# Kernel optimization log

Measured on AMD Instinct MI355X. Metric: run time of the kernel, lower is better.

Reference implementation:

```python
import jax, jax.numpy as jnp
import numpy as np

B, N, DM = 4, 1024, 256
DEPTH, D_STATE, D_CONV, EXPAND = 12, 16, 4, 2
D_INNER = EXPAND * DM
DT_RANK = (DM + 15) // 16
MASKED = 256            # fixed number of masked tokens per row (CLS never masked)
MAX_VIS = N - MASKED    # static visible length -> jit-safe gather/pad
EPS = 1e-5


def setup_inputs() -> dict:
    key = jax.random.key(0)
    ks = jax.random.split(key, 8)
    tokens = jax.random.normal(ks[0], (B, N, DM), jnp.float32)
    # mask: exactly MASKED random positions True per row, among first N-1 (CLS visible)
    def row_mask(k):
        perm = jax.random.permutation(k, N - 1)
        return jnp.zeros((N,), bool).at[perm[:MASKED]].set(True)
    mask = jax.vmap(row_mask)(jax.random.split(ks[1], B))
    sc = 0.02
    L = DEPTH
    in_proj_w = jax.random.normal(ks[2], (L, 2 * D_INNER, DM), jnp.float32) * sc
    conv_w = jax.random.normal(ks[3], (L, D_INNER, D_CONV), jnp.float32) * sc
    conv_b = jnp.zeros((L, D_INNER), jnp.float32)
    x_proj_w = jax.random.normal(ks[4], (L, DT_RANK + 2 * D_STATE, D_INNER), jnp.float32) * sc
    dt_proj_w = jax.random.normal(ks[5], (L, D_INNER, DT_RANK), jnp.float32) * (DT_RANK ** -0.5)
    dt_proj_b = jnp.full((L, D_INNER), float(np.log(np.expm1(0.01))), jnp.float32)  # softplus^-1(0.01)
    A_log = jnp.log(jnp.broadcast_to(jnp.arange(1, D_STATE + 1, dtype=jnp.float32), (L, D_INNER, D_STATE)))
    D_skip = jnp.ones((L, D_INNER), jnp.float32)
    out_proj_w = jax.random.normal(ks[6], (L, DM, D_INNER), jnp.float32) * sc
    norm_w = jnp.ones((L, DM), jnp.float32)
    norm_f_w = jnp.ones((DM,), jnp.float32)
    ln_w = jnp.ones((DM,), jnp.float32)
    ln_b = jnp.zeros((DM,), jnp.float32)
    return dict(tokens=tokens, mask=mask, in_proj_w=in_proj_w, conv_w=conv_w, conv_b=conv_b,
                x_proj_w=x_proj_w, dt_proj_w=dt_proj_w, dt_proj_b=dt_proj_b, A_log=A_log,
                D_skip=D_skip, out_proj_w=out_proj_w, norm_w=norm_w, norm_f_w=norm_f_w,
                ln_w=ln_w, ln_b=ln_b)


def _rmsnorm(x, w):
    return x * jax.lax.rsqrt(jnp.mean(x * x, axis=-1, keepdims=True) + EPS) * w


def _selective_scan(dA, dBu, C):
    # linear recurrence h_t = dA_t * h_{t-1} + dBu_t via associative scan over time
    def comb(l, r):
        return (r[0] * l[0], r[0] * l[1] + r[1])
    _, h = jax.lax.associative_scan(comb, (dA, dBu), axis=1)  # [B,L,d_inner,d_state]
    return jnp.einsum('blds,bls->bld', h, C)


def _mamba(h, p):
    in_w, cw, cb, xw, dtw, dtb, Alog, Dd, ow = p
    L = h.shape[1]
    xz = jnp.einsum('bld,ed->ble', h, in_w)           # [B,L,2*d_inner]
    x, z = jnp.split(xz, 2, axis=-1)
    # causal depthwise conv1d (torch Conv1d, padding=d_conv-1, truncated to L)
    xp = jnp.pad(x, ((0, 0), (D_CONV - 1, 0), (0, 0)))
    x = sum(xp[:, k:k + L, :] * cw[:, k] for k in range(D_CONV)) + cb
    x = jax.nn.silu(x)
    xdbl = jnp.einsum('bld,ed->ble', x, xw)           # [B,L,dt_rank+2*d_state]
    dtr = xdbl[..., :DT_RANK]
    Bm = xdbl[..., DT_RANK:DT_RANK + D_STATE]
    Cm = xdbl[..., DT_RANK + D_STATE:]
    dt = jax.nn.softplus(jnp.einsum('blr,dr->bld', dtr, dtw) + dtb)  # [B,L,d_inner]
    A = -jnp.exp(Alog)                                 # [d_inner,d_state]
    dA = jnp.exp(dt[..., None] * A)                    # [B,L,d_inner,d_state]
    dBu = (dt * x)[..., None] * Bm[:, :, None, :]
    y = _selective_scan(dA, dBu, Cm) + Dd * x
    y = y * jax.nn.silu(z)
    return jnp.einsum('bld,od->blo', y, ow)


def _forward(tokens, mask, in_proj_w, conv_w, conv_b, x_proj_w, dt_proj_w, dt_proj_b,
             A_log, D_skip, out_proj_w, norm_w, norm_f_w, ln_w, ln_b):
    # gather visible tokens, preserving order (stable sort: visible first)
    sort_key = mask.astype(jnp.int32) * N + jnp.arange(N)
    order = jnp.argsort(sort_key, axis=1)[:, :MAX_VIS]           # [B,MAX_VIS]
    vis = jnp.take_along_axis(tokens, order[..., None], axis=1)  # [B,MAX_VIS,DM]

    def step(carry, p):
        hidden, residual = carry
        residual = hidden + residual
        hidden = _mamba(_rmsnorm(residual, p[0]), p[1:])
        return (hidden, residual), None

    layer_params = (norm_w, in_proj_w, conv_w, conv_b, x_proj_w, dt_proj_w, dt_proj_b,
                    A_log, D_skip, out_proj_w)
    (h, r), _ = jax.lax.scan(step, (vis, jnp.zeros_like(vis)), layer_params)
    h = _rmsnorm(h + r, norm_f_w)
    # final nn.LayerNorm
    mu = jnp.mean(h, axis=-1, keepdims=True)
    var = jnp.mean((h - mu) ** 2, axis=-1, keepdims=True)
    h = (h - mu) * jax.lax.rsqrt(var + EPS) * ln_w + ln_b
    return h[:, :-1], h[:, -1]


def reference(tokens, mask, in_proj_w, conv_w, conv_b, x_proj_w, dt_proj_w, dt_proj_b,
              A_log, D_skip, out_proj_w, norm_w, norm_f_w, ln_w, ln_b):
    return _forward(tokens, mask, in_proj_w, conv_w, conv_b, x_proj_w, dt_proj_w, dt_proj_b,
                    A_log, D_skip, out_proj_w, norm_w, norm_f_w, ln_w, ln_b)
```

## Files before the change

kernel.cpp:

```cpp
#include <hip/hip_runtime.h>
#include <stdint.h>

#define B_ 4
#define N_TOK 1024
#define DM 256
#define DEPTH 12
#define DSTATE 16
#define DIN 512
#define LVIS 768
#define MROWS (B_ * LVIS)
#define NCHUNK 64
#define CLEN 12
#define EPS_F 1e-5f
#define YS 520
#define AS_ 264
#define LOG2E 1.4426950408889634f
#define LN2   0.6931471805599453f

typedef __attribute__((ext_vector_type(8))) short s8v;
typedef __attribute__((ext_vector_type(4))) float f4v;

__device__ __forceinline__ float bs2f(uint32_t u) {
  uint32_t x = (u & 0xffffu) << 16;
  float f; __builtin_memcpy(&f, &x, 4); return f;
}
__device__ __forceinline__ uint16_t f2b(float f) {
  uint32_t u; __builtin_memcpy(&u, &f, 4);
  return (uint16_t)((u + 0x7fffu + ((u >> 16) & 1u)) >> 16);
}
__device__ __forceinline__ float exp2_f(float x) {
  float r; asm("v_exp_f32 %0, %1" : "=v"(r) : "v"(x)); return r;
}
__device__ __forceinline__ float log2_f(float x) {
  float r; asm("v_log_f32 %0, %1" : "=v"(r) : "v"(x)); return r;
}
__device__ __forceinline__ float rcp_f(float x) {
  float r; asm("v_rcp_f32 %0, %1" : "=v"(r) : "v"(x)); return r;
}
__device__ __forceinline__ float silu_f(float x) {
  return x * rcp_f(1.f + exp2_f(-x * LOG2E));
}
__device__ __forceinline__ float softplus_f(float x) {
  float t = exp2_f(-fabsf(x) * LOG2E);
  return fmaxf(x, 0.f) + log2_f(1.f + t) * LN2;
}
__device__ __forceinline__ float block_sum256(float v, volatile float* scr) {
  int t = threadIdx.x, lane = t & 63, wid = t >> 6;
#pragma unroll
  for (int o = 32; o > 0; o >>= 1) v += __shfl_down(v, o);
  __syncthreads();
  if (lane == 0) scr[wid] = v;
  __syncthreads();
  return scr[0] + scr[1] + scr[2] + scr[3];
}

__global__ void detect_kernel(const void* mask, const uint32_t* nf, int* flags) {
  __shared__ int cnt[3];
  int t = threadIdx.x;
  if (t < 3) cnt[t] = 0;
  __syncthreads();
  const uint32_t* pi = (const uint32_t*)mask;
  const uint16_t* ph = (const uint16_t*)mask;
  const uint8_t*  pb = (const uint8_t*)mask;
  int c32 = 0, cbf = 0, c8 = 0;
  for (int i = t; i < 1024; i += 256) {
    c32 += (pi[i] != 0u);
    cbf += (ph[i] != 0);
    c8  += (pb[i] != 0);
  }
  atomicAdd(&cnt[0], c32);
  atomicAdd(&cnt[1], cbf);
  atomicAdd(&cnt[2], c8);
  __syncthreads();
  if (t == 0) {
    int f;
    if (cnt[0] == 256) f = 0;
    else if (cnt[1] == 256) f = 2;
    else f = 1;
    flags[0] = f;
    flags[1] = (nf[0] == 0x3F800000u) ? 0 : 1;
  }
}

struct CvtArgs {
  const void* src[13];
  void*       dst[13];
  int         n[13];
  int         isb16[13];
};
__global__ __launch_bounds__(256) void cvt_all_kernel(CvtArgs a, int total,
                                                      const int* __restrict__ flags) {
  int e = blockIdx.x * 256 + threadIdx.x;
  if (e >= total) return;
  int i = 0;
  while (e >= a.n[i]) { e -= a.n[i]; ++i; }
  int srcb16 = flags[1];
  if (a.isb16[i]) {
    uint16_t v = srcb16 ? ((const uint16_t*)a.src[i])[e]
                        : f2b(((const float*)a.src[i])[e]);
    ((uint16_t*)a.dst[i])[e] = v;
  } else {
    float v = srcb16 ? bs2f(((const uint16_t*)a.src[i])[e])
                     : ((const float*)a.src[i])[e];
    ((float*)a.dst[i])[e] = v;
  }
}

__global__ __launch_bounds__(1024) void order_kernel(const void* mask,
                                                     const int* __restrict__ flags,
                                                     int* __restrict__ order) {
  int b = blockIdx.x, i = threadIdx.x;
  int f = flags[0];
  int mv;
  if (f == 0)      mv = (((const uint32_t*)mask)[b * N_TOK + i] != 0u);
  else if (f == 1) mv = (((const uint8_t*)mask)[b * N_TOK + i] != 0);
  else             mv = (((const uint16_t*)mask)[b * N_TOK + i] != 0);
  int vis = !mv;
  unsigned long long mb = __ballot(vis);
  int lane = i & 63, wid = i >> 6;
  int wpre = __popcll(mb & ((1ull << lane) - 1ull));
  __shared__ int wsum[16];
  __shared__ int woff[16];
  if (lane == 0) wsum[wid] = __popcll(mb);
  __syncthreads();
  if (i == 0) { int a = 0; for (int w = 0; w < 16; ++w) { woff[w] = a; a += wsum[w]; } }
  __syncthreads();
  if (vis) {
    int pos = woff[wid] + wpre;
    if (pos < LVIS) order[b * LVIS + pos] = i;
  }
}

__global__ __launch_bounds__(256) void gather_rms_kernel(const void* __restrict__ tokens,
                                                         const int* __restrict__ order,
                                                         const int* __restrict__ flags,
                                                         const float* __restrict__ nw,
                                                         float* __restrict__ residual,
                                                         uint16_t* __restrict__ rmsb16) {
  __shared__ float scr[4];
  int row = blockIdx.x;
  int b = row / LVIS;
  int d = threadIdx.x;
  int idx = order[row];
  size_t src = ((size_t)(b * N_TOK + idx)) * DM + d;
  float v = flags[1] ? bs2f(((const uint16_t*)tokens)[src]) : ((const float*)tokens)[src];
  size_t i = (size_t)row * DM + d;
  residual[i] = v;
  float ss = block_sum256(v * v, scr);
  rmsb16[i] = f2b(v * rsqrtf(ss / DM + EPS_F) * nw[d]);
}

__device__ __forceinline__ size_t cidx(int b, int c, int s, int d) {
  return (((size_t)(b * NCHUNK + c) * 16 + s)) * DIN + d;
}

__global__ __launch_bounds__(1024, 4) void scan1_kernel(
    const uint16_t* __restrict__ rmsb16, const uint16_t* __restrict__ inw,
    const uint16_t* __restrict__ xw,
    const float* __restrict__ cw, const float* __restrict__ cb,
    const float* __restrict__ dtw, const float* __restrict__ dtb,
    const float* __restrict__ Alog, const float* __restrict__ Dsk,
    uint16_t* __restrict__ zh16, float* __restrict__ hend,
    float* __restrict__ pend, float* __restrict__ xdbl_out,
    float* __restrict__ yloc, float* __restrict__ Ssum) {
  __shared__ uint16_t As[16 * AS_];
  __shared__ uint16_t xzl[16 * YS];
  __shared__ float red[8][768];
  __shared__ float xds[CLEN * 48];
  uint16_t* zt = (uint16_t*)red;
  const int t = threadIdx.x;
  const int wv = t >> 6, lane = t & 63;
  const int lm = lane & 15, lq = lane >> 4;
  const int c = blockIdx.x & (NCHUNK - 1);
  const int b = blockIdx.x >> 6;
  const int rowbase = b * LVIS + c * CLEN;
  if (t < 512) {
    int r = t >> 5, seg = t & 31;
    int grow = rowbase - 3 + r;
    if (grow < 0) grow = 0;
    if (grow > MROWS - 1) grow = MROWS - 1;
    *(uint4*)(As + r * AS_ + seg * 8) =
        *(const uint4*)(rmsb16 + (size_t)grow * DM + seg * 8);
  }
  __syncthreads();
  {
    f4v acc[4];
#pragma unroll
    for (int j = 0; j < 4; ++j) acc[j] = (f4v){0.f, 0.f, 0.f, 0.f};
    for (int k0 = 0; k0 < DM; k0 += 32) {
      s8v a = *(const s8v*)(As + lm * AS_ + k0 + lq * 8);
#pragma unroll
      for (int j = 0; j < 4; ++j) {
        int n = (4 * wv + j) * 16 + lm;
        s8v bw = *(const s8v*)(inw + (size_t)n * DM + k0 + lq * 8);
        acc[j] = __builtin_amdgcn_mfma_f32_16x16x32_bf16(a, bw, acc[j], 0, 0, 0);
      }
    }
#pragma unroll
    for (int j = 0; j < 4; ++j) {
      int col = (4 * wv + j) * 16 + lm;
#pragma unroll
      for (int rr = 0; rr < 4; ++rr) {
        int tr = lq * 4 + rr;
        uint16_t v = f2b(acc[j][rr]);
        if (col < 512) xzl[tr * YS + col] = v;
        else           zt[tr * YS + (col - 512)] = v;
      }
    }
  }
  __syncthreads();
  if (t < 768) {
    int r = t >> 6, q = t & 63;
    *(uint4*)(zh16 + (size_t)(rowbase + r) * 512 + q * 8) =
        *(const uint4*)(zt + (3 + r) * YS + q * 8);
  }
  __syncthreads();
  if (wv < 8) {
    f4v acc[3];
#pragma unroll
    for (int j = 0; j < 3; ++j) acc[j] = (f4v){0.f, 0.f, 0.f, 0.f};
    const int l = c * CLEN + lm;
    const bool t3 = l >= 3, t2 = l >= 2, t1 = l >= 1;
#pragma unroll
    for (int ki = 0; ki < 2; ++ki) {
      int kk = wv * 64 + ki * 32 + lq * 8;
      s8v a8 = {0, 0, 0, 0, 0, 0, 0, 0};
      if (lm < CLEN) {
        const s8v zv = {0, 0, 0, 0, 0, 0, 0, 0};
        s8v x0 = *(const s8v*)(xzl + (lm + 3) * YS + kk);
        s8v x1 = t1 ? *(const s8v*)(xzl + (lm + 2) * YS + kk) : zv;
        s8v x2 = t2 ? *(const s8v*)(xzl + (lm + 1) * YS + kk) : zv;
        s8v x3 = t3 ? *(const s8v*)(xzl + (lm + 0) * YS + kk) : zv;
#pragma unroll
        for (int j = 0; j < 8; ++j) {
          int ch = kk + j;
          float4 w = *(const float4*)(cw + ch * 4);
          float a = cb[ch] + bs2f((uint16_t)x3[j]) * w.x +
                    bs2f((uint16_t)x2[j]) * w.y +
                    bs2f((uint16_t)x1[j]) * w.z + bs2f((uint16_t)x0[j]) * w.w;
          a8[j] = (short)f2b(silu_f(a));
        }
      }
#pragma unroll
      for (int j = 0; j < 3; ++j) {
        s8v bb = *(const s8v*)(xw + (size_t)(j * 16 + lm) * DIN + kk);
        acc[j] = __builtin_amdgcn_mfma_f32_16x16x32_bf16(a8, bb, acc[j], 0, 0, 0);
      }
    }
#pragma unroll
    for (int j = 0; j < 3; ++j)
#pragma unroll
      for (int rr = 0; rr < 4; ++rr)
        red[wv][(lq * 4 + rr) * 48 + j * 16 + lm] = acc[j][rr];
  }
  __syncthreads();
  if (t < CLEN * 48) {
    float v = red[0][t] + red[1][t] + red[2][t] + red[3][t] +
              red[4][t] + red[5][t] + red[6][t] + red[7][t];
    xds[t] = v;
    xdbl_out[(size_t)(rowbase + t / 48) * 48 + (t % 48)] = v;
  }
  __syncthreads();
  if (t < DIN) {
    const int d = t;
    float A2[16], dw[16];
    {
      const float4* ap = (const float4*)(Alog + (size_t)d * 16);
      const float4* wp = (const float4*)(dtw + (size_t)d * 16);
#pragma unroll
      for (int q = 0; q < 4; ++q) {
        float4 a4 = ap[q], w4 = wp[q];
        A2[4 * q + 0] = -__expf(a4.x) * LOG2E;
        A2[4 * q + 1] = -__expf(a4.y) * LOG2E;
        A2[4 * q + 2] = -__expf(a4.z) * LOG2E;
        A2[4 * q + 3] = -__expf(a4.w) * LOG2E;
        dw[4 * q + 0] = w4.x; dw[4 * q + 1] = w4.y;
        dw[4 * q + 2] = w4.z; dw[4 * q + 3] = w4.w;
      }
    }
    float dtbv = dtb[d], cbv = cb[d], Dv = Dsk[d];
    float4 cwv = *(const float4*)(cw + d * 4);
    float w3 = 0.f, w2 = 0.f, w1 = 0.f;
    if (c > 0) {
      w3 = bs2f(xzl[0 * YS + d]);
      w2 = bs2f(xzl[1 * YS + d]);
      w1 = bs2f(xzl[2 * YS + d]);
    }
    float h[16];
#pragma unroll
    for (int s = 0; s < 16; ++s) h[s] = 0.f;
    float S = 0.f;
    for (int l = 0; l < CLEN; ++l) {
      float xn = bs2f(xzl[(l + 3) * YS + d]);
      float xv = silu_f(cbv + w3 * cwv.x + w2 * cwv.y + w1 * cwv.z + xn * cwv.w);
      w3 = w2; w2 = w1; w1 = xn;
      const float* xd = xds + l * 48;
      float dtraw = dtbv;
#pragma unroll
      for (int q = 0; q < 16; ++q) dtraw += xd[q] * dw[q];
      float dtv = softplus_f(dtraw);
      float dtx = dtv * xv;
      S += dtv;
      float y = 0.f;
#pragma unroll
      for (int s = 0; s < 16; ++s) {
        float dA = exp2_f(dtv * A2[s]);
        h[s] = dA * h[s] + dtx * xd[16 + s];
        y += h[s] * xd[32 + s];
      }
      size_t oi = (size_t)(rowbase + l) * DIN + d;
      yloc[oi] = y + Dv * xv;
      Ssum[oi] = S;
    }
#pragma unroll
    for (int s = 0; s < 16; ++s) {
      hend[cidx(b, c, s, d)] = h[s];
      pend[cidx(b, c, s, d)] = exp2_f(A2[s] * S);
    }
  }
}

__global__ __launch_bounds__(256) void scan2_kernel(const float* __restrict__ hend,
                                                    const float* __restrict__ pend,
                                                    float* __restrict__ hin) {
  __shared__ float sP[4 * 64];
  __shared__ float sE[4 * 64];
  int t = threadIdx.x;
  int w = t >> 6, lane = t & 63;
  int chain = blockIdx.x * 64 + lane;
  int d = chain & (DIN - 1);
  int s = (chain >> 9) & 15;
  int b = chain >> 13;
  float P = 1.f, E = 0.f;
  float pr[16], hr[16];
#pragma unroll
  for (int i = 0; i < 16; ++i) {
    size_t idx = cidx(b, w * 16 + i, s, d);
    float pv = pend[idx], ev = hend[idx];
    pr[i] = pv; hr[i] = ev;
    E = pv * E + ev;
    P *= pv;
  }
  sP[w * 64 + lane] = P;
  sE[w * 64 + lane] = E;
  __syncthreads();
  float hc = 0.f;
#pragma unroll
  for (int j = 0; j < 3; ++j)
    if (j < w) hc = sP[j * 64 + lane] * hc + sE[j * 64 + lane];
#pragma unroll
  for (int i = 0; i < 16; ++i) {
    hin[cidx(b, w * 16 + i, s, d)] = hc;
    hc = pr[i] * hc + hr[i];
  }
}

__global__ __launch_bounds__(1024, 4) void scan3_fused_kernel(
    const uint16_t* __restrict__ zh16, const float* __restrict__ xdbl,
    const float* __restrict__ Alog, const float* __restrict__ hin,
    const float* __restrict__ yloc, const float* __restrict__ Ssum,
    const uint16_t* __restrict__ W, const float* __restrict__ nw,
    float* __restrict__ residual, uint16_t* __restrict__ rmsb16) {
  __shared__ float xds[CLEN * 48];
  __shared__ uint16_t yml[16 * YS];
  __shared__ float part[16][16];
  __shared__ float scale[16];
  const int t = threadIdx.x;
  const int c = blockIdx.x & (NCHUNK - 1);
  const int b = blockIdx.x >> 6;
  const int rowbase = b * LVIS + c * CLEN;
  if (t < CLEN * 48)
    xds[t] = xdbl[(size_t)(rowbase + t / 48) * 48 + (t % 48)];
  for (int e = t; e < 4 * 512; e += 1024)
    yml[(12 + (e >> 9)) * YS + (e & 511)] = 0;
  __syncthreads();
  if (t < DIN) {
    const int d = t;
    float A2[16];
    {
      const float4* ap = (const float4*)(Alog + (size_t)d * 16);
#pragma unroll
      for (int q = 0; q < 4; ++q) {
        float4 a4 = ap[q];
        A2[4 * q + 0] = -__expf(a4.x) * LOG2E;
        A2[4 * q + 1] = -__expf(a4.y) * LOG2E;
        A2[4 * q + 2] = -__expf(a4.z) * LOG2E;
        A2[4 * q + 3] = -__expf(a4.w) * LOG2E;
      }
    }
    float chin[16];
#pragma unroll
    for (int s = 0; s < 16; ++s) chin[s] = hin[cidx(b, c, s, d)];
    for (int l = 0; l < CLEN; ++l) {
      int row = rowbase + l;
      size_t oi = (size_t)row * DIN + d;
      float S = Ssum[oi];
      float yl = yloc[oi];
      const float* xd = xds + l * 48;
      float carry = 0.f;
#pragma unroll
      for (int s = 0; s < 16; ++s)
        carry += xd[32 + s] * chin[s] * exp2_f(A2[s] * S);
      float zv = bs2f(zh16[(size_t)row * 512 + d]);
      yml[l * YS + d] = f2b((yl + carry) * silu_f(zv));
    }
  }
  __syncthreads();
  {
    const int wv = t >> 6, lane = t & 63;
    const int lm = lane & 15, lq = lane >> 4;
    f4v acc = (f4v){0.f, 0.f, 0.f, 0.f};
    for (int k0 = 0; k0 < DIN; k0 += 32) {
      s8v a = *(const s8v*)(yml + lm * YS + k0 + lq * 8);
      int n = wv * 16 + lm;
      s8v bf = *(const s8v*)(W + (size_t)n * DIN + k0 + lq * 8);
      acc = __builtin_amdgcn_mfma_f32_16x16x32_bf16(a, bf, acc, 0, 0, 0);
    }
    float vv[4];
    float sum[4] = {0.f, 0.f, 0.f, 0.f};
#pragma unroll
    for (int rr = 0; rr < 4; ++rr) {
      int row = lq * 4 + rr;
      if (row < CLEN) {
        int col = wv * 16 + lm;
        float v = acc[rr] + residual[(size_t)(rowbase + row) * DM + col];
        vv[rr] = v;
        sum[rr] += v * v;
      }
    }
#pragma unroll
    for (int rr = 0; rr < 4; ++rr) {
#pragma unroll
      for (int o = 1; o < 16; o <<= 1) sum[rr] += __shfl_xor(sum[rr], o);
    }
    if (lm == 0) {
#pragma unroll
      for (int rr = 0; rr < 4; ++rr) {
        int row = lq * 4 + rr;
        if (row < 16) part[row][wv] = sum[rr];
      }
    }
    __syncthreads();
    if (t < CLEN) {
      float s = 0.f;
#pragma unroll
      for (int w = 0; w < 16; ++w) s += part[t][w];
      scale[t] = rsqrtf(s / DM + EPS_F);
    }
    __syncthreads();
#pragma unroll
    for (int rr = 0; rr < 4; ++rr) {
      int row = lq * 4 + rr;
      if (row < CLEN) {
        float sc = scale[row];
        int col = wv * 16 + lm;
        float v = vv[rr];
        size_t oi = (size_t)(rowbase + row) * DM + col;
        residual[oi] = v;
        rmsb16[oi] = f2b(v * sc * nw[col]);
      }
    }
  }
}

__global__ __launch_bounds__(256) void final_kernel(const float* __restrict__ residual,
                                                    const float* __restrict__ nfw,
                                                    const float* __restrict__ lnw,
                                                    const float* __restrict__ lnb,
                                                    const int* __restrict__ flags,
                                                    void* __restrict__ out) {
  __shared__ float scr[4];
  int row = blockIdx.x, d = threadIdx.x;
  size_t i = (size_t)row * DM + d;
  float v = residual[i];
  float ss = block_sum256(v * v, scr);
  float h = v * rsqrtf(ss / DM + EPS_F) * nfw[d];
  float mu = block_sum256(h, scr) / DM;
  float dv = h - mu;
  float var = block_sum256(dv * dv, scr) / DM;
  float o = dv * rsqrtf(var + EPS_F) * lnw[d] + lnb[d];
  int b = row / LVIS, l = row % LVIS;
  size_t oi = (l < LVIS - 1)
                ? ((size_t)(b * (LVIS - 1) + l) * DM + d)
                : ((size_t)B_ * (LVIS - 1) * DM + (size_t)b * DM + d);
  if (flags[1]) ((uint16_t*)out)[oi] = f2b(o);
  else          ((float*)out)[oi] = o;
}

extern "C" void kernel_launch(void* const* d_in, const int* in_sizes, int n_in,
                              void* d_out, int out_size, void* d_ws, size_t ws_size,
                              hipStream_t stream) {
  char* ws = (char*)d_ws;
  size_t off = 0;
  auto alloc = [&](size_t bytes) -> void* {
    void* p = ws + off;
    off += (bytes + 255) & ~(size_t)255;
    return p;
  };
  const int f32_idx[10] = {3, 4, 6, 7, 8, 9, 11, 12, 13, 14};
  const int b16_idx[3]  = {2, 5, 10};
  float*    f32c[15] = {nullptr};
  uint16_t* b16c[15] = {nullptr};
  for (int j = 0; j < 10; ++j) {
    int i = f32_idx[j];
    f32c[i] = (float*)alloc((size_t)in_sizes[i] * 4);
  }
  for (int j = 0; j < 3; ++j) {
    int i = b16_idx[j];
    b16c[i] = (uint16_t*)alloc((size_t)in_sizes[i] * 2);
  }
  float*    residual = (float*)alloc((size_t)MROWS * DM * 4);
  uint16_t* rmsb16   = (uint16_t*)alloc((size_t)MROWS * DM * 2);
  uint16_t* zh16     = (uint16_t*)alloc((size_t)MROWS * 512 * 2);
  float*    xdbl     = (float*)alloc((size_t)MROWS * 48 * 4);
  float*    hend     = (float*)alloc((size_t)B_ * NCHUNK * DIN * 16 * 4);
  float*    pend     = (float*)alloc((size_t)B_ * NCHUNK * DIN * 16 * 4);
  float*    hin      = (float*)alloc((size_t)B_ * NCHUNK * DIN * 16 * 4);
  float*    yloc     = (float*)alloc((size_t)MROWS * DIN * 4);
  float*    Ssum     = (float*)alloc((size_t)MROWS * DIN * 4);
  int*      order    = (int*)alloc((size_t)B_ * LVIS * 4);
  int*      flags    = (int*)alloc(256);

  detect_kernel<<<1, 256, 0, stream>>>(d_in[1], (const uint32_t*)d_in[12], flags);

  CvtArgs ca;
  int total = 0, slot = 0;
  for (int j = 0; j < 3; ++j) {
    int i = b16_idx[j];
    ca.src[slot] = d_in[i]; ca.dst[slot] = b16c[i];
    ca.n[slot] = in_sizes[i]; ca.isb16[slot] = 1;
    total += in_sizes[i]; ++slot;
  }
  for (int j = 0; j < 10; ++j) {
    int i = f32_idx[j];
    ca.src[slot] = d_in[i]; ca.dst[slot] = f32c[i];
    ca.n[slot] = in_sizes[i]; ca.isb16[slot] = 0;
    total += in_sizes[i]; ++slot;
  }
  cvt_all_kernel<<<(total + 255) / 256, 256, 0, stream>>>(ca, total, flags);

  const uint16_t* in_w   = b16c[2];
  const float*    conv_w = f32c[3];
  const float*    conv_b = f32c[4];
  const uint16_t* x_w    = b16c[5];
  const float*    dt_w   = f32c[6];
  const float*    dt_b   = f32c[7];
  const float*    A_log  = f32c[8];
  const float*    D_skip = f32c[9];
  const uint16_t* out_w  = b16c[10];
  const float*    norm_w = f32c[11];
  const float*    norm_f = f32c[12];
  const float*    ln_w   = f32c[13];
  const float*    ln_b   = f32c[14];

  order_kernel<<<B_, 1024, 0, stream>>>(d_in[1], flags, order);
  gather_rms_kernel<<<MROWS, 256, 0, stream>>>(d_in[0], order, flags, norm_w,
                                               residual, rmsb16);

  for (int L = 0; L < DEPTH; ++L) {
    scan1_kernel<<<B_ * NCHUNK, 1024, 0, stream>>>(
        rmsb16, in_w + (size_t)L * 1024 * DM, x_w + (size_t)L * 48 * DIN,
        conv_w + (size_t)L * DIN * 4, conv_b + (size_t)L * DIN,
        dt_w + (size_t)L * DIN * 16, dt_b + (size_t)L * DIN,
        A_log + (size_t)L * DIN * 16, D_skip + (size_t)L * DIN,
        zh16, hend, pend, xdbl, yloc, Ssum);
    scan2_kernel<<<(B_ * 16 * DIN * 4) / 256, 256, 0, stream>>>(hend, pend, hin);
    int Lnext = (L + 1 < DEPTH) ? (L + 1) : L;
    scan3_fused_kernel<<<B_ * NCHUNK, 1024, 0, stream>>>(
        zh16, xdbl, A_log + (size_t)L * DIN * 16, hin, yloc, Ssum,
        out_w + (size_t)L * DM * DIN, norm_w + (size_t)Lnext * DM,
        residual, rmsb16);
  }

  final_kernel<<<MROWS, 256, 0, stream>>>(residual, norm_f, ln_w, ln_b,
                                          flags, d_out);
}
```

Measured before the change: 788.5 us.

## Split scan states across thread pairs, recompute chunk decay, fuse final norm into last layer

In scan1, each channel's 16 SSM states are now split across two threads, so all 1024 threads run the scan instead of 512; the partial y values are combined with a lane shuffle. The pend buffer is removed, and scan2 recomputes each chunk's decay from Ssum and A_log. The xdbl buffer now stores only the 16 C columns. The final RMSNorm+LayerNorm kernel is folded into a templated last-layer variant of scan3, which drops one launch and one pass over the residual. The costs are extra exp work in scan2, a duplicated dt projection in each thread pair, and more syncs in the last layer.

```diff
diff --git a/kernel.cpp b/kernel.cpp
--- a/kernel.cpp
+++ b/kernel.cpp
@@ -161,8 +161,8 @@
     const float* __restrict__ dtw, const float* __restrict__ dtb,
     const float* __restrict__ Alog, const float* __restrict__ Dsk,
     uint16_t* __restrict__ zh16, float* __restrict__ hend,
-    float* __restrict__ pend, float* __restrict__ xdbl_out,
-    float* __restrict__ yloc, float* __restrict__ Ssum) {
+    float* __restrict__ xdbl_out, float* __restrict__ yloc,
+    float* __restrict__ Ssum) {
   __shared__ uint16_t As[16 * AS_];
   __shared__ uint16_t xzl[16 * YS];
   __shared__ float red[8][768];
@@ -258,22 +258,29 @@
     float v = red[0][t] + red[1][t] + red[2][t] + red[3][t] +
               red[4][t] + red[5][t] + red[6][t] + red[7][t];
     xds[t] = v;
-    xdbl_out[(size_t)(rowbase + t / 48) * 48 + (t % 48)] = v;
-  }
-  __syncthreads();
-  if (t < DIN) {
-    const int d = t;
-    float A2[16], dw[16];
+    int k = t % 48;
+    if (k >= 32)
+      xdbl_out[(size_t)(rowbase + t / 48) * 16 + (k - 32)] = v;
+  }
+  __syncthreads();
+  {
+    const int d = t >> 1;
+    const int s0 = (t & 1) * 8;
+    float A2[8], dw[16];
     {
-      const float4* ap = (const float4*)(Alog + (size_t)d * 16);
+      const float4* ap = (const float4*)(Alog + (size_t)d * 16 + s0);
       const float4* wp = (const float4*)(dtw + (size_t)d * 16);
 #pragma unroll
-      for (int q = 0; q < 4; ++q) {
-        float4 a4 = ap[q], w4 = wp[q];
+      for (int q = 0; q < 2; ++q) {
+        float4 a4 = ap[q];
         A2[4 * q + 0] = -__expf(a4.x) * LOG2E;
         A2[4 * q + 1] = -__expf(a4.y) * LOG2E;
         A2[4 * q + 2] = -__expf(a4.z) * LOG2E;
         A2[4 * q + 3] = -__expf(a4.w) * LOG2E;
+      }
+#pragma unroll
+      for (int q = 0; q < 4; ++q) {
+        float4 w4 = wp[q];
         dw[4 * q + 0] = w4.x; dw[4 * q + 1] = w4.y;
         dw[4 * q + 2] = w4.z; dw[4 * q + 3] = w4.w;
       }
@@ -286,9 +293,9 @@
       w2 = bs2f(xzl[1 * YS + d]);
       w1 = bs2f(xzl[2 * YS + d]);
     }
-    float h[16];
-#pragma unroll
-    for (int s = 0; s < 16; ++s) h[s] = 0.f;
+    float h[8];
+#pragma unroll
+    for (int i = 0; i < 8; ++i) h[i] = 0.f;
     float S = 0.f;
     for (int l = 0; l < CLEN; ++l) {
       float xn = bs2f(xzl[(l + 3) * YS + d]);
@@ -303,25 +310,27 @@
       S += dtv;
       float y = 0.f;
 #pragma unroll
-      for (int s = 0; s < 16; ++s) {
-        float dA = exp2_f(dtv * A2[s]);
-        h[s] = dA * h[s] + dtx * xd[16 + s];
-        y += h[s] * xd[32 + s];
-      }
-      size_t oi = (size_t)(rowbase + l) * DIN + d;
-      yloc[oi] = y + Dv * xv;
-      Ssum[oi] = S;
-    }
-#pragma unroll
-    for (int s = 0; s < 16; ++s) {
-      hend[cidx(b, c, s, d)] = h[s];
-      pend[cidx(b, c, s, d)] = exp2_f(A2[s] * S);
-    }
+      for (int i = 0; i < 8; ++i) {
+        float dA = exp2_f(dtv * A2[i]);
+        h[i] = dA * h[i] + dtx * xd[16 + s0 + i];
+        y += h[i] * xd[32 + s0 + i];
+      }
+      y += __shfl_xor(y, 1);
+      if (!(t & 1)) {
+        size_t oi = (size_t)(rowbase + l) * DIN + d;
+        yloc[oi] = y + Dv * xv;
+        Ssum[oi] = S;
+      }
+    }
+#pragma unroll
+    for (int i = 0; i < 8; ++i)
+      hend[cidx(b, c, s0 + i, d)] = h[i];
   }
 }
 
 __global__ __launch_bounds__(256) void scan2_kernel(const float* __restrict__ hend,
-                                                    const float* __restrict__ pend,
+                                                    const float* __restrict__ Ssum,
+                                                    const float* __restrict__ Alog,
                                                     float* __restrict__ hin) {
   __shared__ float sP[4 * 64];
   __shared__ float sE[4 * 64];
@@ -331,12 +340,15 @@
   int d = chain & (DIN - 1);
   int s = (chain >> 9) & 15;
   int b = chain >> 13;
+  float A2v = -__expf(Alog[(size_t)d * 16 + s]) * LOG2E;
   float P = 1.f, E = 0.f;
   float pr[16], hr[16];
 #pragma unroll
   for (int i = 0; i < 16; ++i) {
-    size_t idx = cidx(b, w * 16 + i, s, d);
-    float pv = pend[idx], ev = hend[idx];
+    int cc = w * 16 + i;
+    float Send = Ssum[(size_t)(b * LVIS + cc * CLEN + CLEN - 1) * DIN + d];
+    float pv = exp2_f(A2v * Send);
+    float ev = hend[cidx(b, cc, s, d)];
     pr[i] = pv; hr[i] = ev;
     E = pv * E + ev;
     P *= pv;
@@ -355,13 +367,17 @@
   }
 }
 
+template <int LAST>
 __global__ __launch_bounds__(1024, 4) void scan3_fused_kernel(
     const uint16_t* __restrict__ zh16, const float* __restrict__ xdbl,
     const float* __restrict__ Alog, const float* __restrict__ hin,
     const float* __restrict__ yloc, const float* __restrict__ Ssum,
     const uint16_t* __restrict__ W, const float* __restrict__ nw,
-    float* __restrict__ residual, uint16_t* __restrict__ rmsb16) {
-  __shared__ float xds[CLEN * 48];
+    float* __restrict__ residual, uint16_t* __restrict__ rmsb16,
+    const float* __restrict__ nfw, const float* __restrict__ lnw,
+    const float* __restrict__ lnb, const int* __restrict__ flags,
+    void* __restrict__ out) {
+  __shared__ float xds[CLEN * 16];
   __shared__ uint16_t yml[16 * YS];
   __shared__ float part[16][16];
   __shared__ float scale[16];
@@ -369,8 +385,8 @@
   const int c = blockIdx.x & (NCHUNK - 1);
   const int b = blockIdx.x >> 6;
   const int rowbase = b * LVIS + c * CLEN;
-  if (t < CLEN * 48)
-    xds[t] = xdbl[(size_t)(rowbase + t / 48) * 48 + (t % 48)];
+  if (t < CLEN * 16)
+    xds[t] = xdbl[(size_t)(rowbase + t / 16) * 16 + (t % 16)];
   for (int e = t; e < 4 * 512; e += 1024)
     yml[(12 + (e >> 9)) * YS + (e & 511)] = 0;
   __syncthreads();
@@ -396,11 +412,11 @@
       size_t oi = (size_t)row * DIN + d;
       float S = Ssum[oi];
       float yl = yloc[oi];
-      const float* xd = xds + l * 48;
+      const float* xd = xds + l * 16;
       float carry = 0.f;
 #pragma unroll
       for (int s = 0; s < 16; ++s)
-        carry += xd[32 + s] * chin[s] * exp2_f(A2[s] * S);
+        carry += xd[s] * chin[s] * exp2_f(A2[s] * S);
       float zv = bs2f(zh16[(size_t)row * 512 + d]);
       yml[l * YS + d] = f2b((yl + carry) * silu_f(zv));
     }
@@ -409,10 +425,11 @@
   {
     const int wv = t >> 6, lane = t & 63;
     const int lm = lane & 15, lq = lane >> 4;
+    const int col = wv * 16 + lm;
     f4v acc = (f4v){0.f, 0.f, 0.f, 0.f};
     for (int k0 = 0; k0 < DIN; k0 += 32) {
       s8v a = *(const s8v*)(yml + lm * YS + k0 + lq * 8);
-      int n = wv * 16 + lm;
+      int n = col;
       s8v bf = *(const s8v*)(W + (size_t)n * DIN + k0 + lq * 8);
       acc = __builtin_amdgcn_mfma_f32_16x16x32_bf16(a, bf, acc, 0, 0, 0);
     }
@@ -422,7 +439,6 @@
     for (int rr = 0; rr < 4; ++rr) {
       int row = lq * 4 + rr;
       if (row < CLEN) {
-        int col = wv * 16 + lm;
         float v = acc[rr] + residual[(size_t)(rowbase + row) * DM + col];
         vv[rr] = v;
         sum[rr] += v * v;
@@ -448,43 +464,99 @@
       scale[t] = rsqrtf(s / DM + EPS_F);
     }
     __syncthreads();
-#pragma unroll
-    for (int rr = 0; rr < 4; ++rr) {
-      int row = lq * 4 + rr;
-      if (row < CLEN) {
-        float sc = scale[row];
-        int col = wv * 16 + lm;
-        float v = vv[rr];
-        size_t oi = (size_t)(rowbase + row) * DM + col;
-        residual[oi] = v;
-        rmsb16[oi] = f2b(v * sc * nw[col]);
-      }
-    }
-  }
-}
-
-__global__ __launch_bounds__(256) void final_kernel(const float* __restrict__ residual,
-                                                    const float* __restrict__ nfw,
-                                                    const float* __restrict__ lnw,
-                                                    const float* __restrict__ lnb,
-                                                    const int* __restrict__ flags,
-                                                    void* __restrict__ out) {
-  __shared__ float scr[4];
-  int row = blockIdx.x, d = threadIdx.x;
-  size_t i = (size_t)row * DM + d;
-  float v = residual[i];
-  float ss = block_sum256(v * v, scr);
-  float h = v * rsqrtf(ss / DM + EPS_F) * nfw[d];
-  float mu = block_sum256(h, scr) / DM;
-  float dv = h - mu;
-  float var = block_sum256(dv * dv, scr) / DM;
-  float o = dv * rsqrtf(var + EPS_F) * lnw[d] + lnb[d];
-  int b = row / LVIS, l = row % LVIS;
-  size_t oi = (l < LVIS - 1)
-                ? ((size_t)(b * (LVIS - 1) + l) * DM + d)
-                : ((size_t)B_ * (LVIS - 1) * DM + (size_t)b * DM + d);
-  if (flags[1]) ((uint16_t*)out)[oi] = f2b(o);
-  else          ((float*)out)[oi] = o;
+    if (!LAST) {
+#pragma unroll
+      for (int rr = 0; rr < 4; ++rr) {
+        int row = lq * 4 + rr;
+        if (row < CLEN) {
+          float sc = scale[row];
+          float v = vv[rr];
+          size_t oi = (size_t)(rowbase + row) * DM + col;
+          residual[oi] = v;
+          rmsb16[oi] = f2b(v * sc * nw[col]);
+        }
+      }
+    } else {
+      float hv[4];
+      float mu[4] = {0.f, 0.f, 0.f, 0.f};
+#pragma unroll
+      for (int rr = 0; rr < 4; ++rr) {
+        int row = lq * 4 + rr;
+        hv[rr] = 0.f;
+        if (row < CLEN) {
+          hv[rr] = vv[rr] * scale[row] * nfw[col];
+          mu[rr] = hv[rr];
+        }
+      }
+#pragma unroll
+      for (int rr = 0; rr < 4; ++rr) {
+#pragma unroll
+        for (int o = 1; o < 16; o <<= 1) mu[rr] += __shfl_xor(mu[rr], o);
+      }
+      __syncthreads();
+      if (lm == 0) {
+#pragma unroll
+        for (int rr = 0; rr < 4; ++rr) {
+          int row = lq * 4 + rr;
+          if (row < 16) part[row][wv] = mu[rr];
+        }
+      }
+      __syncthreads();
+      if (t < CLEN) {
+        float s = 0.f;
+#pragma unroll
+        for (int w = 0; w < 16; ++w) s += part[t][w];
+        scale[t] = s / DM;
+      }
+      __syncthreads();
+      float dv_[4];
+      float va[4] = {0.f, 0.f, 0.f, 0.f};
+#pragma unroll
+      for (int rr = 0; rr < 4; ++rr) {
+        int row = lq * 4 + rr;
+        dv_[rr] = 0.f;
+        if (row < CLEN) {
+          dv_[rr] = hv[rr] - scale[row];
+          va[rr] = dv_[rr] * dv_[rr];
+        }
+      }
+#pragma unroll
+      for (int rr = 0; rr < 4; ++rr) {
+#pragma unroll
+        for (int o = 1; o < 16; o <<= 1) va[rr] += __shfl_xor(va[rr], o);
+      }
+      __syncthreads();
+      if (lm == 0) {
+#pragma unroll
+        for (int rr = 0; rr < 4; ++rr) {
+          int row = lq * 4 + rr;
+          if (row < 16) part[row][wv] = va[rr];
+        }
+      }
+      __syncthreads();
+      if (t < CLEN) {
+        float s = 0.f;
+#pragma unroll
+        for (int w = 0; w < 16; ++w) s += part[t][w];
+        scale[t] = rsqrtf(s / DM + EPS_F);
+      }
+      __syncthreads();
+      int f1 = flags[1];
+#pragma unroll
+      for (int rr = 0; rr < 4; ++rr) {
+        int row = lq * 4 + rr;
+        if (row < CLEN) {
+          float o = dv_[rr] * scale[row] * lnw[col] + lnb[col];
+          int l2 = c * CLEN + row;
+          size_t oi = (l2 < LVIS - 1)
+                        ? ((size_t)(b * (LVIS - 1) + l2) * DM + col)
+                        : ((size_t)B_ * (LVIS - 1) * DM + (size_t)b * DM + col);
+          if (f1) ((uint16_t*)out)[oi] = f2b(o);
+          else    ((float*)out)[oi] = o;
+        }
+      }
+    }
+  }
 }
 
 extern "C" void kernel_launch(void* const* d_in, const int* in_sizes, int n_in,
@@ -512,9 +584,8 @@
   float*    residual = (float*)alloc((size_t)MROWS * DM * 4);
   uint16_t* rmsb16   = (uint16_t*)alloc((size_t)MROWS * DM * 2);
   uint16_t* zh16     = (uint16_t*)alloc((size_t)MROWS * 512 * 2);
-  float*    xdbl     = (float*)alloc((size_t)MROWS * 48 * 4);
+  float*    xdbl     = (float*)alloc((size_t)MROWS * 16 * 4);
   float*    hend     = (float*)alloc((size_t)B_ * NCHUNK * DIN * 16 * 4);
-  float*    pend     = (float*)alloc((size_t)B_ * NCHUNK * DIN * 16 * 4);
   float*    hin      = (float*)alloc((size_t)B_ * NCHUNK * DIN * 16 * 4);
   float*    yloc     = (float*)alloc((size_t)MROWS * DIN * 4);
   float*    Ssum     = (float*)alloc((size_t)MROWS * DIN * 4);
@@ -563,15 +634,20 @@
         conv_w + (size_t)L * DIN * 4, conv_b + (size_t)L * DIN,
         dt_w + (size_t)L * DIN * 16, dt_b + (size_t)L * DIN,
         A_log + (size_t)L * DIN * 16, D_skip + (size_t)L * DIN,
-        zh16, hend, pend, xdbl, yloc, Ssum);
-    scan2_kernel<<<(B_ * 16 * DIN * 4) / 256, 256, 0, stream>>>(hend, pend, hin);
+        zh16, hend, xdbl, yloc, Ssum);
+    scan2_kernel<<<(B_ * 16 * DIN * 4) / 256, 256, 0, stream>>>(
+        hend, Ssum, A_log + (size_t)L * DIN * 16, hin);
     int Lnext = (L + 1 < DEPTH) ? (L + 1) : L;
-    scan3_fused_kernel<<<B_ * NCHUNK, 1024, 0, stream>>>(
-        zh16, xdbl, A_log + (size_t)L * DIN * 16, hin, yloc, Ssum,
-        out_w + (size_t)L * DM * DIN, norm_w + (size_t)Lnext * DM,
-        residual, rmsb16);
-  }
-
-  final_kernel<<<MROWS, 256, 0, stream>>>(residual, norm_f, ln_w, ln_b,
-                                          flags, d_out);
-}
+    if (L + 1 < DEPTH) {
+      scan3_fused_kernel<0><<<B_ * NCHUNK, 1024, 0, stream>>>(
+          zh16, xdbl, A_log + (size_t)L * DIN * 16, hin, yloc, Ssum,
+          out_w + (size_t)L * DM * DIN, norm_w + (size_t)Lnext * DM,
+          residual, rmsb16, norm_f, ln_w, ln_b, flags, d_out);
+    } else {
+      scan3_fused_kernel<1><<<B_ * NCHUNK, 1024, 0, stream>>>(
+          zh16, xdbl, A_log + (size_t)L * DIN * 16, hin, yloc, Ssum,
+          out_w + (size_t)L * DM * DIN, norm_w + (size_t)Lnext * DM,
+          residual, rmsb16, norm_f, ln_w, ln_b, flags, d_out);
+    }
+  }
+}
```

Measured after the change: 786.7 us. No clear change (-0.2%).
